# Performance work log

Hardware: AMD Instinct MI355X
Metric: run time of the kernel (lower is better)

The kernel has to match this reference:

```python
import jax, jax.numpy as jnp
import numpy as np

N_V, N_H, T, B = 1024, 512, 128, 256


def setup_inputs() -> dict:
    key = jax.random.key(0)
    k = jax.random.split(key, 3)
    v_data = (jax.random.uniform(k[0], (N_V, T, B)) < 0.5).astype(jnp.float32)  # binary visibles
    W = 0.01 * jax.random.normal(k[1], (N_H, N_V), jnp.float32)
    U = 0.01 * jax.random.normal(k[2], (N_H, N_H), jnp.float32)
    b_h = jnp.zeros((N_H,), jnp.float32)
    b_init = jnp.zeros((N_H,), jnp.float32)
    b_v = jnp.zeros((N_V,), jnp.float32)
    return {"v_data": v_data, "W": W, "U": U, "b_h": b_h, "b_init": b_init,
            "b_v": b_v, "CDk": 2}


def _sample_r_over_time(v, W, U, b_h, b_init):
    # v: (V,T,B) -> r: (H,T,B). Sequential mean-field recurrence over T
    # (RTRBM._sample_r_given_v_over_time: t=0 uses b_init and U=0, t>0 uses U,b_h).
    Wv = jnp.einsum('hv,vtb->thb', W, v)  # (T,H,B)
    r0 = jax.nn.sigmoid(Wv[0] + b_init[:, None])

    def step(r_lag, wv_t):
        r_t = jax.nn.sigmoid(wv_t + U @ r_lag + b_h[:, None])
        return r_t, r_t

    _, rs = jax.lax.scan(step, r0, Wv[1:])
    r = jnp.concatenate([r0[None], rs], axis=0)  # (T,H,B)
    return jnp.transpose(r, (1, 0, 2))  # (H,T,B)


def _parallel_r(v, r_lagged, W, U, b_h, b_init):
    # RTRBM._parallel_sample_r_h_given_v probabilities; v:(V,T,B), r_lagged:(H,T,B)
    r0 = jax.nn.sigmoid(jnp.einsum('hv,vb->hb', W, v[:, 0]) + b_init[:, None])
    rr = jax.nn.sigmoid(jnp.einsum('hv,vtb->htb', W, v[:, 1:])
                        + jnp.einsum('hr,rtb->htb', U, r_lagged[:, :-1])
                        + b_h[:, None, None])
    return jnp.concatenate([r0[:, None], rr], axis=1)  # (H,T,B)


def reference(v_data, W, U, b_h, b_init, b_v, CDk):
    key = jax.random.key(42)
    r_data = _sample_r_over_time(v_data, W, U, b_h, b_init)
    key, sk = jax.random.split(key)
    h_model = jax.random.bernoulli(sk, _parallel_r(v_data, r_data, W, U, b_h, b_init)).astype(v_data.dtype)
    for _ in range(CDk - 1):  # CD-k Gibbs chain (CDk is a concrete Python int)
        key, k1, k2 = jax.random.split(key, 3)
        v_prob = jax.nn.sigmoid(jnp.einsum('hv,htb->vtb', W, h_model) + b_v[:, None, None])
        v_model = jax.random.bernoulli(k1, v_prob).astype(v_data.dtype)
        h_model = jax.random.bernoulli(k2, _parallel_r(v_model, r_data, W, U, b_h, b_init)).astype(v_data.dtype)
    key, kf = jax.random.split(key)
    v_model = jax.random.bernoulli(
        kf, jax.nn.sigmoid(jnp.einsum('hv,htb->vtb', W, h_model) + b_v[:, None, None])
    ).astype(v_data.dtype)
    return (v_model, r_data)
```

## Files before the change

kernel.cpp:

```cpp
#include <hip/hip_runtime.h>
#include <hip/hip_bf16.h>
#include <stdint.h>

typedef unsigned long long u64;
typedef uint32_t u32;
typedef __attribute__((ext_vector_type(8))) short bf16x8;
typedef __attribute__((ext_vector_type(4))) float f32x4;

#define NV 1024
#define NH 512
#define TT 128
#define BB 256
#define TBsz (TT*BB)
#define HTBsz (NH*TBsz)
#define VTBsz (NV*TBsz)
#define NWV (NV/64)
#define NWH (NH/64)
#define QCAP 1048576u
#define DELTA 5e-4

__host__ __device__ inline void tf2x32(uint32_t k0, uint32_t k1,
                                       uint32_t x0, uint32_t x1,
                                       uint32_t& o0, uint32_t& o1) {
  const uint32_t ks2 = k0 ^ k1 ^ 0x1BD11BDAu;
#define ROTL(x,d) (((x)<<(d))|((x)>>(32-(d))))
#define RND(r) { x0 += x1; x1 = ROTL(x1,r); x1 ^= x0; }
  x0 += k0;  x1 += k1;
  RND(13) RND(15) RND(26) RND(6)
  x0 += k1;  x1 += ks2 + 1u;
  RND(17) RND(29) RND(16) RND(24)
  x0 += ks2; x1 += k0 + 2u;
  RND(13) RND(15) RND(26) RND(6)
  x0 += k0;  x1 += k1 + 3u;
  RND(17) RND(29) RND(16) RND(24)
  x0 += k1;  x1 += ks2 + 4u;
  RND(13) RND(15) RND(26) RND(6)
  x0 += ks2; x1 += k0 + 5u;
  o0 = x0; o1 = x1;
#undef RND
#undef ROTL
}

__device__ inline double tf_uniform64(uint32_t k0, uint32_t k1, uint32_t i) {
  uint32_t o0, o1;
  tf2x32(k0, k1, 0u, i, o0, o1);
  uint32_t bits = o0 ^ o1;
  uint32_t fb = (bits >> 9) | 0x3f800000u;
  float f = __uint_as_float(fb) - 1.0f;
  return (double)f;
}

__device__ inline double sigmoid64(double x) { return 1.0 / (1.0 + exp(-x)); }

__device__ inline void bfsplit(float w, ushort& b1o, ushort& b2o) {
  __hip_bfloat16 b1 = __float2bfloat16(w);
  float r = w - __bfloat162float(b1);
  __hip_bfloat16 b2 = __float2bfloat16(r);
  b1o = *reinterpret_cast<ushort*>(&b1);
  b2o = *reinterpret_cast<ushort*>(&b2);
}

__global__ __launch_bounds__(256) void kprepWall(const float* __restrict__ W,
                                                 double* __restrict__ W64,
                                                 ushort* __restrict__ A1,
                                                 ushort* __restrict__ A2,
                                                 ushort* __restrict__ AW1,
                                                 ushort* __restrict__ AW2) {
  int idx = blockIdx.x * 256 + threadIdx.x;
  W64[idx] = (double)W[idx];
  {
    int i    = idx & 7;
    int lane = (idx >> 3) & 63;
    int ks   = (idx >> 9) & 15;
    int vt   = idx >> 13;
    int h = ks*32 + ((lane >> 4) << 3) + i;
    int v = vt*16 + (lane & 15);
    bfsplit(W[(size_t)h*NV + v], A1[idx], A2[idx]);
  }
  {
    int i    = idx & 7;
    int lane = (idx >> 3) & 63;
    int kt   = (idx >> 9) & 31;
    int ht   = idx >> 14;
    int h = ht*16 + (lane & 15);
    int v = kt*32 + ((lane >> 4) << 3) + i;
    bfsplit(W[(size_t)h*NV + v], AW1[idx], AW2[idx]);
  }
}

__global__ __launch_bounds__(256) void kprepUall(const float* __restrict__ U,
                                                 double* __restrict__ U64,
                                                 float4* __restrict__ UB,
                                                 ushort* __restrict__ AU1,
                                                 ushort* __restrict__ AU2) {
  int idx = blockIdx.x * 256 + threadIdx.x;
  U64[idx] = (double)U[idx];
  {
    int i    = idx & 7;
    int lane = (idx >> 3) & 63;
    int kt   = (idx >> 9) & 15;
    int ht   = idx >> 13;
    int h = ht*16 + (lane & 15);
    int r = kt*32 + ((lane >> 4) << 3) + i;
    bfsplit(U[(size_t)h*NH + r], AU1[idx], AU2[idx]);
  }
  if (idx < NH*NH/4) {
    int r4 = idx / NH;
    int h  = idx % NH;
    const float* __restrict__ p = U + (size_t)h*NH + r4*4;
    UB[idx] = make_float4(p[0], p[1], p[2], p[3]);
  }
}

__global__ __launch_bounds__(256) void kpack_f32(const float* __restrict__ in,
                                                 u64* __restrict__ out) {
  int tb = blockIdx.x * 256 + threadIdx.x;
  for (int w = 0; w < NWV; ++w) {
    u64 m = 0;
    #pragma unroll 8
    for (int j = 0; j < 64; ++j)
      m |= (u64)(in[(size_t)(w*64 + j)*TBsz + tb] != 0.0f ? 1 : 0) << j;
    out[(size_t)tb*NWV + w] = m;
  }
}

__global__ __launch_bounds__(256) void kWv(const u64* __restrict__ vb,
                                           const double* __restrict__ W64,
                                           double* __restrict__ WvT) {
  const int HM = 8;
  int t  = blockIdx.x / (NH/HM);
  int h0 = (blockIdx.x % (NH/HM)) * HM;
  int tb = t*BB + threadIdx.x;
  u64 m[NWV];
  #pragma unroll
  for (int w = 0; w < NWV; ++w) m[w] = vb[(size_t)tb*NWV + w];
  double acc[HM];
  #pragma unroll
  for (int i = 0; i < HM; ++i) acc[i] = 0.0;
  const double2* __restrict__ W2 = (const double2*)W64;
  for (int w = 0; w < NWV; ++w) {
    u64 mw = m[w];
    #pragma unroll 8
    for (int j2 = 0; j2 < 32; ++j2) {
      double bd0 = (double)((unsigned)((mw >> (2*j2+0)) & 1ull));
      double bd1 = (double)((unsigned)((mw >> (2*j2+1)) & 1ull));
      int vi = w*32 + j2;
      #pragma unroll
      for (int i = 0; i < HM; ++i) {
        double2 wv = W2[(size_t)(h0+i)*(NV/2) + vi];
        acc[i] = fma(bd0, wv.x, acc[i]);
        acc[i] = fma(bd1, wv.y, acc[i]);
      }
    }
  }
  #pragma unroll
  for (int i = 0; i < HM; ++i)
    WvT[(size_t)tb*NH + h0 + i] = acc[i];
}

__global__ __launch_bounds__(512) void krecur(const double* __restrict__ WvT,
                                              const float4* __restrict__ UB,
                                              const float* __restrict__ bh,
                                              const float* __restrict__ binit,
                                              double* __restrict__ rT) {
  __shared__ double rA[2][NH];
  const int b = blockIdx.x;
  const int h = threadIdx.x;
  const double bhd = (double)bh[h];
  double p = sigmoid64(WvT[(size_t)b*NH + h] + (double)binit[h]);
  rA[0][h] = p;
  rT[(size_t)b*NH + h] = p;
  __syncthreads();
  int cur = 0;
  for (int t = 1; t < TT; ++t) {
    double acc = WvT[((size_t)t*BB + b)*NH + h];
    double a0=0, a1=0, a2=0, a3=0;
    const double2* __restrict__ rA2 = (const double2*)rA[cur];
    #pragma unroll 4
    for (int r = 0; r < NH; r += 4) {
      float4 u4 = UB[(size_t)(r >> 2)*NH + h];
      double2 q01 = rA2[(r>>1)+0];
      double2 q23 = rA2[(r>>1)+1];
      a0 = fma((double)u4.x, q01.x, a0);
      a1 = fma((double)u4.y, q01.y, a1);
      a2 = fma((double)u4.z, q23.x, a2);
      a3 = fma((double)u4.w, q23.y, a3);
    }
    p = sigmoid64((acc + ((a0+a1)+(a2+a3))) + bhd);
    rA[cur ^ 1][h] = p;
    rT[((size_t)t*BB + b)*NH + h] = p;
    __syncthreads();
    cur ^= 1;
  }
}

__global__ __launch_bounds__(256) void ktrans_s(const double* __restrict__ rT,
                                                float* __restrict__ out_r,
                                                uint8_t* __restrict__ hbytes,
                                                u32 k0, u32 k1) {
  __shared__ double lds[32][33];
  int t  = blockIdx.x;
  int h0 = blockIdx.y * 32;
  int b0 = blockIdx.z * 32;
  int tx = threadIdx.x & 31;
  int ty = threadIdx.x >> 5;
  #pragma unroll
  for (int i = 0; i < 4; ++i) {
    int row = ty*4 + i;
    lds[row][tx] = rT[((size_t)t*BB + b0 + row)*NH + h0 + tx];
  }
  __syncthreads();
  #pragma unroll
  for (int i = 0; i < 4; ++i) {
    int row = ty*4 + i;
    out_r[(size_t)(h0+row)*TBsz + (size_t)t*BB + b0 + tx] = (float)lds[tx][row];
  }
  if (threadIdx.x < 128) {
    int tbr = threadIdx.x >> 2;
    int bix = threadIdx.x & 3;
    int tb  = t*BB + b0 + tbr;
    unsigned byte = 0;
    #pragma unroll
    for (int j = 0; j < 8; ++j) {
      int hrel = bix*8 + j;
      double p = lds[tbr][hrel];
      double u = tf_uniform64(k0, k1, (u32)((h0 + hrel)*TBsz + tb));
      byte |= (u < p) ? (1u << j) : 0u;
    }
    hbytes[(size_t)tb*(NH/8) + (h0 >> 3) + bix] = (uint8_t)byte;
  }
}

__global__ __launch_bounds__(256) void kvisM(
    const ushort* __restrict__ A1, const ushort* __restrict__ A2,
    const float* __restrict__ bv, const u64* __restrict__ hbits,
    u64* __restrict__ vbits, float* __restrict__ vf,
    u32* __restrict__ queue, u32* __restrict__ cnt, u32 k0, u32 k1) {
  __shared__ ushort Blds[128*512];
  __shared__ u64 sbits[128];
  int tb0 = blockIdx.x * 128;
  int tid = threadIdx.x;
  {
    int c  = tid & 127;
    int hs = tid >> 7;
    const u64* hp = hbits + (size_t)(tb0 + c)*NWH + hs*4;
    #pragma unroll
    for (int w = 0; w < 4; ++w) {
      u64 mm = hp[w];
      int kbase = hs*256 + w*64;
      #pragma unroll
      for (int j2 = 0; j2 < 32; ++j2) {
        int k = kbase + 2*j2;
        u32 val = (u32)((mm >> (2*j2)) & 1ull) * 0x3F80u
                | (u32)((mm >> (2*j2+1)) & 1ull) * 0x3F800000u;
        int blk = (k >> 3) ^ (c & 7);
        *(u32*)&Blds[c*512 + (blk << 3) + (k & 7)] = val;
      }
    }
  }
  __syncthreads();
  int wv = tid >> 6, l = tid & 63;
  int wr = wv >> 1, wc = wv & 1;
  for (int vblk = 0; vblk < 16; ++vblk) {
    f32x4 acc[2][4];
    #pragma unroll
    for (int m = 0; m < 2; ++m)
      #pragma unroll
      for (int n = 0; n < 4; ++n) acc[m][n] = (f32x4){0.f,0.f,0.f,0.f};
    for (int ks = 0; ks < 16; ++ks) {
      bf16x8 bf[4];
      #pragma unroll
      for (int n = 0; n < 4; ++n) {
        int col = wc*64 + n*16 + (l & 15);
        int k = ks*32 + ((l >> 4) << 3);
        int blk = (k >> 3) ^ (col & 7);
        bf[n] = *(const bf16x8*)&Blds[col*512 + (blk << 3)];
      }
      #pragma unroll
      for (int m = 0; m < 2; ++m) {
        int vt = vblk*4 + wr*2 + m;
        size_t abase = (((size_t)vt*16 + ks)*64 + l)*8;
        bf16x8 a1 = *(const bf16x8*)&A1[abase];
        bf16x8 a2 = *(const bf16x8*)&A2[abase];
        #pragma unroll
        for (int n = 0; n < 4; ++n) {
          acc[m][n] = __builtin_amdgcn_mfma_f32_16x16x32_bf16(a1, bf[n], acc[m][n], 0,0,0);
          acc[m][n] = __builtin_amdgcn_mfma_f32_16x16x32_bf16(a2, bf[n], acc[m][n], 0,0,0);
        }
      }
    }
    int v0 = vblk * 64;
    u64 mask[4] = {0,0,0,0};
    #pragma unroll
    for (int n = 0; n < 4; ++n) {
      int col = wc*64 + n*16 + (l & 15);
      int tb = tb0 + col;
      #pragma unroll
      for (int m = 0; m < 2; ++m) {
        #pragma unroll
        for (int r = 0; r < 4; ++r) {
          int vrel = wr*32 + m*16 + ((l >> 4) << 2) + r;
          int v = v0 + vrel;
          float p = 1.f / (1.f + __expf(-(acc[m][n][r] + bv[v])));
          size_t o = (size_t)v*TBsz + tb;
          double u = tf_uniform64(k0, k1, (u32)o);
          double diff = (double)p - u;
          unsigned smp = diff > 0.0 ? 1u : 0u;
          if (fabs(diff) < DELTA) {
            u32 s = atomicAdd(cnt, 1u);
            if (s < QCAP) queue[s] = (u32)o;
          }
          if (smp) mask[n] |= 1ull << vrel;
          if (vf) vf[o] = (float)smp;
        }
      }
    }
    if (vbits) {
      __syncthreads();
      if (tid < 128) sbits[tid] = 0;
      __syncthreads();
      #pragma unroll
      for (int n = 0; n < 4; ++n) {
        int col = wc*64 + n*16 + (l & 15);
        atomicOr(&sbits[col], mask[n]);
      }
      __syncthreads();
      if (tid < 128)
        vbits[(size_t)(tb0 + tid)*NWV + vblk] = sbits[tid];
    }
  }
}

__global__ __launch_bounds__(256) void khidM(
    const ushort* __restrict__ AW1, const ushort* __restrict__ AW2,
    const ushort* __restrict__ AU1, const ushort* __restrict__ AU2,
    const float* __restrict__ bh, const float* __restrict__ binit,
    const u64* __restrict__ vbits, const float* __restrict__ r32,
    u64* __restrict__ h2bits, u32* __restrict__ queue,
    u32* __restrict__ cnt, u32 k0, u32 k1) {
  __shared__ ushort Blds[64*512];
  int nblk = blockIdx.x & 511;
  int hblk = blockIdx.x >> 9;
  int tb0 = nblk * 64, h0 = hblk * 64;
  int t = tb0 >> 8;
  int tid = threadIdx.x;
  int wv = tid >> 6, l = tid & 63;
  int wr = wv >> 1, wc = wv & 1;
  f32x4 acc[2][2];
  #pragma unroll
  for (int m = 0; m < 2; ++m)
    #pragma unroll
    for (int n = 0; n < 2; ++n) acc[m][n] = (f32x4){0.f,0.f,0.f,0.f};

  for (int q = 0; q < 2; ++q) {
    {
      int c = tid >> 2, seg = tid & 3;
      const u64* vp = vbits + (size_t)(tb0 + c)*NWV + q*8 + seg*2;
      #pragma unroll
      for (int half = 0; half < 2; ++half) {
        u64 mm = vp[half];
        int kbase = seg*128 + half*64;
        #pragma unroll
        for (int j2 = 0; j2 < 32; ++j2) {
          int k = kbase + 2*j2;
          u32 val = (u32)((mm >> (2*j2)) & 1ull) * 0x3F80u
                  | (u32)((mm >> (2*j2+1)) & 1ull) * 0x3F800000u;
          int blk = (k >> 3) ^ (c & 7);
          *(u32*)&Blds[c*512 + (blk << 3) + (k & 7)] = val;
        }
      }
    }
    __syncthreads();
    for (int ks = 0; ks < 16; ++ks) {
      int kt = q*16 + ks;
      bf16x8 bf[2];
      #pragma unroll
      for (int n = 0; n < 2; ++n) {
        int col = wc*32 + n*16 + (l & 15);
        int k = ks*32 + ((l >> 4) << 3);
        int blk = (k >> 3) ^ (col & 7);
        bf[n] = *(const bf16x8*)&Blds[col*512 + (blk << 3)];
      }
      #pragma unroll
      for (int m = 0; m < 2; ++m) {
        int ht = hblk*4 + wr*2 + m;
        size_t abase = (((size_t)ht*32 + kt)*64 + l)*8;
        bf16x8 a1 = *(const bf16x8*)&AW1[abase];
        bf16x8 a2 = *(const bf16x8*)&AW2[abase];
        #pragma unroll
        for (int n = 0; n < 2; ++n) {
          acc[m][n] = __builtin_amdgcn_mfma_f32_16x16x32_bf16(a1, bf[n], acc[m][n], 0,0,0);
          acc[m][n] = __builtin_amdgcn_mfma_f32_16x16x32_bf16(a2, bf[n], acc[m][n], 0,0,0);
        }
      }
    }
    __syncthreads();
  }

  if (t > 0) {
    int tbl0 = tb0 - 256;
    for (int pl = 0; pl < 2; ++pl) {
      {
        int c  = tid & 63;
        int q4 = tid >> 6;
        const float* __restrict__ rp = r32 + tbl0 + c;
        for (int rr = 0; rr < 128; ++rr) {
          int r = q4*128 + rr;
          float x = rp[(size_t)r*TBsz];
          __hip_bfloat16 b1 = __float2bfloat16(x);
          ushort ub;
          if (pl == 0) {
            ub = *reinterpret_cast<ushort*>(&b1);
          } else {
            float res = x - __bfloat162float(b1);
            __hip_bfloat16 b2 = __float2bfloat16(res);
            ub = *reinterpret_cast<ushort*>(&b2);
          }
          int blk = (r >> 3) ^ (c & 7);
          Blds[c*512 + (blk << 3) + (r & 7)] = ub;
        }
      }
      __syncthreads();
      for (int ks = 0; ks < 16; ++ks) {
        bf16x8 bf[2];
        #pragma unroll
        for (int n = 0; n < 2; ++n) {
          int col = wc*32 + n*16 + (l & 15);
          int k = ks*32 + ((l >> 4) << 3);
          int blk = (k >> 3) ^ (col & 7);
          bf[n] = *(const bf16x8*)&Blds[col*512 + (blk << 3)];
        }
        #pragma unroll
        for (int m = 0; m < 2; ++m) {
          int ht = hblk*4 + wr*2 + m;
          size_t abase = (((size_t)ht*16 + ks)*64 + l)*8;
          bf16x8 a1 = *(const bf16x8*)&AU1[abase];
          bf16x8 a2 = *(const bf16x8*)&AU2[abase];
          #pragma unroll
          for (int n = 0; n < 2; ++n) {
            acc[m][n] = __builtin_amdgcn_mfma_f32_16x16x32_bf16(a1, bf[n], acc[m][n], 0,0,0);
            acc[m][n] = __builtin_amdgcn_mfma_f32_16x16x32_bf16(a2, bf[n], acc[m][n], 0,0,0);
          }
        }
      }
      __syncthreads();
    }
  }

  const float* __restrict__ bias = (t > 0) ? bh : binit;
  u64 mask[2] = {0, 0};
  int coln[2];
  #pragma unroll
  for (int n = 0; n < 2; ++n) {
    int col = wc*32 + n*16 + (l & 15);
    coln[n] = col;
    int tb = tb0 + col;
    #pragma unroll
    for (int m = 0; m < 2; ++m) {
      #pragma unroll
      for (int r = 0; r < 4; ++r) {
        int hrel = wr*32 + m*16 + ((l >> 4) << 2) + r;
        int h = h0 + hrel;
        float p = 1.f / (1.f + __expf(-(acc[m][n][r] + bias[h])));
        size_t o = (size_t)h*TBsz + tb;
        double u = tf_uniform64(k0, k1, (u32)o);
        double diff = (double)p - u;
        unsigned smp = diff > 0.0 ? 1u : 0u;
        if (fabs(diff) < DELTA) {
          u32 s = atomicAdd(cnt, 1u);
          if (s < QCAP) queue[s] = (u32)o;
        }
        if (smp) mask[n] |= 1ull << hrel;
      }
    }
  }
  __syncthreads();
  u64* sbits = (u64*)Blds;
  if (tid < 64) sbits[tid] = 0;
  __syncthreads();
  atomicOr(&sbits[coln[0]], mask[0]);
  atomicOr(&sbits[coln[1]], mask[1]);
  __syncthreads();
  if (tid < 64)
    h2bits[(size_t)(tb0 + tid)*NWH + hblk] = sbits[tid];
}

__global__ __launch_bounds__(256) void kvis_fix(
    const float* __restrict__ W, const float* __restrict__ bv,
    const u64* __restrict__ hbits, u64* __restrict__ fixbits,
    float* __restrict__ vf, const u32* __restrict__ queue,
    const u32* __restrict__ cnt, u32 k0, u32 k1) {
  u32 n = *cnt; if (n > QCAP) n = QCAP;
  for (u32 q = blockIdx.x*256 + threadIdx.x; q < n; q += gridDim.x*256) {
    u32 o = queue[q];
    u32 v = o / TBsz, tb = o % TBsz;
    double a0=0, a1=0, a2=0, a3=0;
    for (int w = 0; w < NWH; ++w) {
      u64 mw = hbits[(size_t)tb*NWH + w];
      for (int j = 0; j < 64; j += 4) {
        if ((mw >> (j+0)) & 1ull) a0 += (double)W[(size_t)(w*64+j+0)*NV + v];
        if ((mw >> (j+1)) & 1ull) a1 += (double)W[(size_t)(w*64+j+1)*NV + v];
        if ((mw >> (j+2)) & 1ull) a2 += (double)W[(size_t)(w*64+j+2)*NV + v];
        if ((mw >> (j+3)) & 1ull) a3 += (double)W[(size_t)(w*64+j+3)*NV + v];
      }
    }
    double p = sigmoid64(((a0+a1)+(a2+a3)) + (double)bv[v]);
    double u = tf_uniform64(k0, k1, o);
    unsigned smp = (u < p) ? 1u : 0u;
    if (vf) vf[o] = (float)smp;
    if (fixbits) {
      size_t wi = (size_t)tb*NWV + (v >> 6);
      unsigned bit = v & 63u;
      unsigned cur = (unsigned)((fixbits[wi] >> bit) & 1ull);
      if (cur != smp) atomicXor(&fixbits[wi], 1ull << bit);
    }
  }
}

__global__ __launch_bounds__(256) void khid_fix(
    const u64* __restrict__ vbits, const float* __restrict__ W,
    const double* __restrict__ U64, const float* __restrict__ bh,
    const float* __restrict__ binit, const double* __restrict__ rT,
    u64* __restrict__ fixbits, const u32* __restrict__ queue,
    const u32* __restrict__ cnt, u32 k0, u32 k1) {
  u32 n = *cnt; if (n > QCAP) n = QCAP;
  for (u32 q = blockIdx.x*256 + threadIdx.x; q < n; q += gridDim.x*256) {
    u32 o = queue[q];
    u32 h = o / TBsz, tb = o % TBsz;
    u32 t = tb / BB, b = tb % BB;
    double a0=0, a1=0, a2=0, a3=0;
    for (int w = 0; w < NWV; ++w) {
      u64 mw = vbits[(size_t)tb*NWV + w];
      for (int j = 0; j < 64; j += 4) {
        if ((mw >> (j+0)) & 1ull) a0 += (double)W[(size_t)h*NV + w*64+j+0];
        if ((mw >> (j+1)) & 1ull) a1 += (double)W[(size_t)h*NV + w*64+j+1];
        if ((mw >> (j+2)) & 1ull) a2 += (double)W[(size_t)h*NV + w*64+j+2];
        if ((mw >> (j+3)) & 1ull) a3 += (double)W[(size_t)h*NV + w*64+j+3];
      }
    }
    double logit = (a0+a1) + (a2+a3);
    if (t > 0) {
      const double* __restrict__ rp = rT + ((size_t)(t-1)*BB + b)*NH;
      const double* __restrict__ Ur = U64 + (size_t)h*NH;
      double u0=0, u1=0, u2=0, u3=0;
      for (int r = 0; r < NH; r += 4) {
        u0 = fma(Ur[r+0], rp[r+0], u0);
        u1 = fma(Ur[r+1], rp[r+1], u1);
        u2 = fma(Ur[r+2], rp[r+2], u2);
        u3 = fma(Ur[r+3], rp[r+3], u3);
      }
      logit = (logit + ((u0+u1)+(u2+u3))) + (double)bh[h];
    } else {
      logit += (double)binit[h];
    }
    double p = sigmoid64(logit);
    double u = tf_uniform64(k0, k1, o);
    unsigned smp = (u < p) ? 1u : 0u;
    size_t wi = (size_t)tb*NWH + (h >> 6);
    unsigned bit = h & 63u;
    unsigned cur = (unsigned)((fixbits[wi] >> bit) & 1ull);
    if (cur != smp) atomicXor(&fixbits[wi], 1ull << bit);
  }
}

extern "C" void kernel_launch(void* const* d_in, const int* in_sizes, int n_in,
                              void* d_out, int out_size, void* d_ws, size_t ws_size,
                              hipStream_t stream) {
  const float* vd    = (const float*)d_in[0];
  const float* W     = (const float*)d_in[1];
  const float* U     = (const float*)d_in[2];
  const float* bh    = (const float*)d_in[3];
  const float* binit = (const float*)d_in[4];
  const float* bv    = (const float*)d_in[5];

  float* out_v = (float*)d_out;
  float* out_r = (float*)d_out + VTBsz;
  double* WvT = (double*)d_out;

  char* w = (char*)d_ws;
  double* rT    = (double*)w;  w += (size_t)HTBsz*8;
  u64* vdbits   = (u64*)w;     w += (size_t)TBsz*NWV*8;
  u64* v1bits   = (u64*)w;     w += (size_t)TBsz*NWV*8;
  u64* h1bits   = (u64*)w;     w += (size_t)TBsz*NWH*8;
  u64* h2bits   = (u64*)w;     w += (size_t)TBsz*NWH*8;
  double* W64   = (double*)w;  w += (size_t)NH*NV*8;
  double* U64   = (double*)w;  w += (size_t)NH*NH*8;
  float4* UB    = (float4*)w;  w += (size_t)NH*NH*4;
  ushort* A1    = (ushort*)w;  w += (size_t)NH*NV*2;
  ushort* A2    = (ushort*)w;  w += (size_t)NH*NV*2;
  ushort* AW1   = (ushort*)w;  w += (size_t)NH*NV*2;
  ushort* AW2   = (ushort*)w;  w += (size_t)NH*NV*2;
  ushort* AU1   = (ushort*)w;  w += (size_t)NH*NH*2;
  ushort* AU2   = (ushort*)w;  w += (size_t)NH*NH*2;
  u32* q0       = (u32*)w;     w += (size_t)QCAP*4;
  u32* q1       = (u32*)w;     w += (size_t)QCAP*4;
  u32* q2       = (u32*)w;     w += (size_t)QCAP*4;
  u32* cnt      = (u32*)w;     w += 256;
  (void)ws_size; (void)in_sizes; (void)n_in; (void)out_size;

  uint32_t ka0,ka1, sk0,sk1;
  tf2x32(0u,42u, 0u,0u, ka0,ka1);
  tf2x32(0u,42u, 0u,1u, sk0,sk1);
  uint32_t kb0,kb1, k10,k11, k20,k21;
  tf2x32(ka0,ka1, 0u,0u, kb0,kb1);
  tf2x32(ka0,ka1, 0u,1u, k10,k11);
  tf2x32(ka0,ka1, 0u,2u, k20,k21);
  uint32_t kc0,kc1, kf0,kf1;
  tf2x32(kb0,kb1, 0u,0u, kc0,kc1);
  tf2x32(kb0,kb1, 0u,1u, kf0,kf1);

  hipMemsetAsync(cnt, 0, 3*sizeof(u32), stream);

  kprepWall<<<(NH*NV)/256, 256, 0, stream>>>(W, W64, A1, A2, AW1, AW2);
  kprepUall<<<(NH*NH)/256, 256, 0, stream>>>(U, U64, UB, AU1, AU2);
  kpack_f32<<<TBsz/256, 256, 0, stream>>>(vd, vdbits);

  kWv<<<TT*(NH/8), 256, 0, stream>>>(vdbits, W64, WvT);

  krecur<<<BB, NH, 0, stream>>>(WvT, UB, bh, binit, rT);

  ktrans_s<<<dim3(TT, NH/32, BB/32), 256, 0, stream>>>(rT, out_r,
                                                       (uint8_t*)h1bits, sk0, sk1);

  kvisM<<<TBsz/128, 256, 0, stream>>>(A1, A2, bv, h1bits, v1bits, nullptr,
                                      q0, cnt+0, k10, k11);
  kvis_fix<<<128, 256, 0, stream>>>(W, bv, h1bits, v1bits, nullptr,
                                    q0, cnt+0, k10, k11);

  khidM<<<8*512, 256, 0, stream>>>(AW1, AW2, AU1, AU2, bh, binit,
                                   v1bits, out_r, h2bits, q1, cnt+1, k20, k21);
  khid_fix<<<128, 256, 0, stream>>>(v1bits, W, U64, bh, binit, rT,
                                    h2bits, q1, cnt+1, k20, k21);

  kvisM<<<TBsz/128, 256, 0, stream>>>(A1, A2, bv, h2bits, nullptr, out_v,
                                      q2, cnt+2, kf0, kf1);
  kvis_fix<<<128, 256, 0, stream>>>(W, bv, h2bits, nullptr, out_v,
                                    q2, cnt+2, kf0, kf1);
}
```

Before: 5.144 ms.

## Transpose W for coalesced fp64 Wv, widen pack grid, pad LDS rows

The fp64 W·v kernel is rewritten to read a transposed W, so that each thread computes two hidden units for one (t,b) column using coalesced double2 loads. The prep kernel builds this transposed copy. The bit-packing kernel now splits work across visible words to get more parallelism. LDS row strides in the MFMA kernels are padded from 512 to 528 to reduce bank conflicts, and the fix-up kernels run with twice as many blocks. The padding increases LDS use, which may lower occupancy.

Result: slower. 8.112 ms (+57.7%).

```diff
diff --git a/kernel.cpp b/kernel.cpp
--- a/kernel.cpp
+++ b/kernel.cpp
@@ -18,6 +18,8 @@
 #define NWH (NH/64)
 #define QCAP 1048576u
 #define DELTA 5e-4
+#define BSTv 528
+#define BSTh 528
 
 __host__ __device__ inline void tf2x32(uint32_t k0, uint32_t k1,
                                        uint32_t x0, uint32_t x1,
@@ -61,13 +63,17 @@
 }
 
 __global__ __launch_bounds__(256) void kprepWall(const float* __restrict__ W,
-                                                 double* __restrict__ W64,
+                                                 double* __restrict__ W64T,
                                                  ushort* __restrict__ A1,
                                                  ushort* __restrict__ A2,
                                                  ushort* __restrict__ AW1,
                                                  ushort* __restrict__ AW2) {
   int idx = blockIdx.x * 256 + threadIdx.x;
-  W64[idx] = (double)W[idx];
+  {
+    int v = idx >> 9;
+    int h = idx & 511;
+    W64T[idx] = (double)W[(size_t)h*NV + v];
+  }
   {
     int i    = idx & 7;
     int lane = (idx >> 3) & 63;
@@ -114,48 +120,49 @@
 
 __global__ __launch_bounds__(256) void kpack_f32(const float* __restrict__ in,
                                                  u64* __restrict__ out) {
-  int tb = blockIdx.x * 256 + threadIdx.x;
-  for (int w = 0; w < NWV; ++w) {
-    u64 m = 0;
-    #pragma unroll 8
-    for (int j = 0; j < 64; ++j)
-      m |= (u64)(in[(size_t)(w*64 + j)*TBsz + tb] != 0.0f ? 1 : 0) << j;
-    out[(size_t)tb*NWV + w] = m;
-  }
-}
-
-__global__ __launch_bounds__(256) void kWv(const u64* __restrict__ vb,
-                                           const double* __restrict__ W64,
-                                           double* __restrict__ WvT) {
-  const int HM = 8;
-  int t  = blockIdx.x / (NH/HM);
-  int h0 = (blockIdx.x % (NH/HM)) * HM;
-  int tb = t*BB + threadIdx.x;
+  int bw = blockIdx.x >> 7;
+  int tb = (blockIdx.x & 127) * 256 + threadIdx.x;
+  u64 m = 0;
+  #pragma unroll 8
+  for (int j = 0; j < 64; ++j)
+    m |= (u64)(in[(size_t)(bw*64 + j)*TBsz + tb] != 0.0f ? 1 : 0) << j;
+  out[(size_t)tb*NWV + bw] = m;
+}
+
+__global__ __launch_bounds__(256) void kWv2(const u64* __restrict__ vb,
+                                            const double* __restrict__ W64T,
+                                            double* __restrict__ WvT) {
+  int tb = blockIdx.x;
+  int h2 = threadIdx.x;
   u64 m[NWV];
   #pragma unroll
   for (int w = 0; w < NWV; ++w) m[w] = vb[(size_t)tb*NWV + w];
-  double acc[HM];
-  #pragma unroll
-  for (int i = 0; i < HM; ++i) acc[i] = 0.0;
-  const double2* __restrict__ W2 = (const double2*)W64;
+  double a0=0, a1=0, a2=0, a3=0;
+  double b0=0, b1=0, b2=0, b3=0;
+  const double2* __restrict__ WT2 = (const double2*)W64T;
   for (int w = 0; w < NWV; ++w) {
     u64 mw = m[w];
-    #pragma unroll 8
-    for (int j2 = 0; j2 < 32; ++j2) {
-      double bd0 = (double)((unsigned)((mw >> (2*j2+0)) & 1ull));
-      double bd1 = (double)((unsigned)((mw >> (2*j2+1)) & 1ull));
-      int vi = w*32 + j2;
-      #pragma unroll
-      for (int i = 0; i < HM; ++i) {
-        double2 wv = W2[(size_t)(h0+i)*(NV/2) + vi];
-        acc[i] = fma(bd0, wv.x, acc[i]);
-        acc[i] = fma(bd1, wv.y, acc[i]);
-      }
-    }
-  }
-  #pragma unroll
-  for (int i = 0; i < HM; ++i)
-    WvT[(size_t)tb*NH + h0 + i] = acc[i];
+    #pragma unroll 4
+    for (int j = 0; j < 64; j += 4) {
+      double d0 = (double)((u32)((mw >> (j+0)) & 1ull));
+      double d1 = (double)((u32)((mw >> (j+1)) & 1ull));
+      double d2 = (double)((u32)((mw >> (j+2)) & 1ull));
+      double d3 = (double)((u32)((mw >> (j+3)) & 1ull));
+      size_t base = (size_t)(w*64 + j)*(NH/2) + h2;
+      double2 w0 = WT2[base + 0*(NH/2)];
+      double2 w1 = WT2[base + 1*(NH/2)];
+      double2 w2 = WT2[base + 2*(NH/2)];
+      double2 w3 = WT2[base + 3*(NH/2)];
+      a0 = fma(d0, w0.x, a0);  b0 = fma(d0, w0.y, b0);
+      a1 = fma(d1, w1.x, a1);  b1 = fma(d1, w1.y, b1);
+      a2 = fma(d2, w2.x, a2);  b2 = fma(d2, w2.y, b2);
+      a3 = fma(d3, w3.x, a3);  b3 = fma(d3, w3.y, b3);
+    }
+  }
+  double2 o;
+  o.x = (a0+a1) + (a2+a3);
+  o.y = (b0+b1) + (b2+b3);
+  ((double2*)(WvT + (size_t)tb*NH))[h2] = o;
 }
 
 __global__ __launch_bounds__(512) void krecur(const double* __restrict__ WvT,
@@ -236,7 +243,7 @@
     const float* __restrict__ bv, const u64* __restrict__ hbits,
     u64* __restrict__ vbits, float* __restrict__ vf,
     u32* __restrict__ queue, u32* __restrict__ cnt, u32 k0, u32 k1) {
-  __shared__ ushort Blds[128*512];
+  __shared__ ushort Blds[128*BSTv];
   __shared__ u64 sbits[128];
   int tb0 = blockIdx.x * 128;
   int tid = threadIdx.x;
@@ -254,7 +261,7 @@
         u32 val = (u32)((mm >> (2*j2)) & 1ull) * 0x3F80u
                 | (u32)((mm >> (2*j2+1)) & 1ull) * 0x3F800000u;
         int blk = (k >> 3) ^ (c & 7);
-        *(u32*)&Blds[c*512 + (blk << 3) + (k & 7)] = val;
+        *(u32*)&Blds[c*BSTv + (blk << 3) + (k & 7)] = val;
       }
     }
   }
@@ -274,7 +281,7 @@
         int col = wc*64 + n*16 + (l & 15);
         int k = ks*32 + ((l >> 4) << 3);
         int blk = (k >> 3) ^ (col & 7);
-        bf[n] = *(const bf16x8*)&Blds[col*512 + (blk << 3)];
+        bf[n] = *(const bf16x8*)&Blds[col*BSTv + (blk << 3)];
       }
       #pragma unroll
       for (int m = 0; m < 2; ++m) {
@@ -338,7 +345,7 @@
     const u64* __restrict__ vbits, const float* __restrict__ r32,
     u64* __restrict__ h2bits, u32* __restrict__ queue,
     u32* __restrict__ cnt, u32 k0, u32 k1) {
-  __shared__ ushort Blds[64*512];
+  __shared__ ushort Blds[64*BSTh];
   int nblk = blockIdx.x & 511;
   int hblk = blockIdx.x >> 9;
   int tb0 = nblk * 64, h0 = hblk * 64;
@@ -366,7 +373,7 @@
           u32 val = (u32)((mm >> (2*j2)) & 1ull) * 0x3F80u
                   | (u32)((mm >> (2*j2+1)) & 1ull) * 0x3F800000u;
           int blk = (k >> 3) ^ (c & 7);
-          *(u32*)&Blds[c*512 + (blk << 3) + (k & 7)] = val;
+          *(u32*)&Blds[c*BSTh + (blk << 3) + (k & 7)] = val;
         }
       }
     }
@@ -379,7 +386,7 @@
         int col = wc*32 + n*16 + (l & 15);
         int k = ks*32 + ((l >> 4) << 3);
         int blk = (k >> 3) ^ (col & 7);
-        bf[n] = *(const bf16x8*)&Blds[col*512 + (blk << 3)];
+        bf[n] = *(const bf16x8*)&Blds[col*BSTh + (blk << 3)];
       }
       #pragma unroll
       for (int m = 0; m < 2; ++m) {
@@ -417,7 +424,7 @@
             ub = *reinterpret_cast<ushort*>(&b2);
           }
           int blk = (r >> 3) ^ (c & 7);
-          Blds[c*512 + (blk << 3) + (r & 7)] = ub;
+          Blds[c*BSTh + (blk << 3) + (r & 7)] = ub;
         }
       }
       __syncthreads();
@@ -428,7 +435,7 @@
           int col = wc*32 + n*16 + (l & 15);
           int k = ks*32 + ((l >> 4) << 3);
           int blk = (k >> 3) ^ (col & 7);
-          bf[n] = *(const bf16x8*)&Blds[col*512 + (blk << 3)];
+          bf[n] = *(const bf16x8*)&Blds[col*BSTh + (blk << 3)];
         }
         #pragma unroll
         for (int m = 0; m < 2; ++m) {
@@ -583,7 +590,7 @@
   u64* v1bits   = (u64*)w;     w += (size_t)TBsz*NWV*8;
   u64* h1bits   = (u64*)w;     w += (size_t)TBsz*NWH*8;
   u64* h2bits   = (u64*)w;     w += (size_t)TBsz*NWH*8;
-  double* W64   = (double*)w;  w += (size_t)NH*NV*8;
+  double* W64T  = (double*)w;  w += (size_t)NH*NV*8;
   double* U64   = (double*)w;  w += (size_t)NH*NH*8;
   float4* UB    = (float4*)w;  w += (size_t)NH*NH*4;
   ushort* A1    = (ushort*)w;  w += (size_t)NH*NV*2;
@@ -611,11 +618,11 @@
 
   hipMemsetAsync(cnt, 0, 3*sizeof(u32), stream);
 
-  kprepWall<<<(NH*NV)/256, 256, 0, stream>>>(W, W64, A1, A2, AW1, AW2);
+  kprepWall<<<(NH*NV)/256, 256, 0, stream>>>(W, W64T, A1, A2, AW1, AW2);
   kprepUall<<<(NH*NH)/256, 256, 0, stream>>>(U, U64, UB, AU1, AU2);
-  kpack_f32<<<TBsz/256, 256, 0, stream>>>(vd, vdbits);
-
-  kWv<<<TT*(NH/8), 256, 0, stream>>>(vdbits, W64, WvT);
+  kpack_f32<<<2048, 256, 0, stream>>>(vd, vdbits);
+
+  kWv2<<<TBsz, 256, 0, stream>>>(vdbits, W64T, WvT);
 
   krecur<<<BB, NH, 0, stream>>>(WvT, UB, bh, binit, rT);
 
@@ -624,16 +631,16 @@
 
   kvisM<<<TBsz/128, 256, 0, stream>>>(A1, A2, bv, h1bits, v1bits, nullptr,
                                       q0, cnt+0, k10, k11);
-  kvis_fix<<<128, 256, 0, stream>>>(W, bv, h1bits, v1bits, nullptr,
+  kvis_fix<<<256, 256, 0, stream>>>(W, bv, h1bits, v1bits, nullptr,
                                     q0, cnt+0, k10, k11);
 
   khidM<<<8*512, 256, 0, stream>>>(AW1, AW2, AU1, AU2, bh, binit,
                                    v1bits, out_r, h2bits, q1, cnt+1, k20, k21);
-  khid_fix<<<128, 256, 0, stream>>>(v1bits, W, U64, bh, binit, rT,
+  khid_fix<<<256, 256, 0, stream>>>(v1bits, W, U64, bh, binit, rT,
                                     h2bits, q1, cnt+1, k20, k21);
 
   kvisM<<<TBsz/128, 256, 0, stream>>>(A1, A2, bv, h2bits, nullptr, out_v,
                                       q2, cnt+2, kf0, kf1);
-  kvis_fix<<<128, 256, 0, stream>>>(W, bv, h2bits, nullptr, out_v,
+  kvis_fix<<<256, 256, 0, stream>>>(W, bv, h2bits, nullptr, out_v,
                                     q2, cnt+2, kf0, kf1);
 }
```
